# Kernel optimization log

Hardware: AMD Instinct MI355X
Metric: run time of the kernel (lower is better)

Reference implementation:

```python
import jax, jax.numpy as jnp
import numpy as np

N = 100000      # nodes (single ntype)
F_IN = 128
F_OUT = 128
R = 3           # relations
E = 262144      # edges per relation
LRELU_SLOPE = 0.2


def setup_inputs() -> dict:
    key = jax.random.key(0)
    ks = jax.random.split(key, 6)
    x = jax.random.normal(ks[0], (N, F_IN), jnp.float32)
    src = jax.random.randint(ks[1], (R, E), 0, N)
    dst = jax.random.randint(ks[2], (R, E), 0, N)
    # attention: Linear(2*in_feat, 1) per relation
    att_w = jax.random.normal(ks[3], (R, 2 * F_IN, 1), jnp.float32) * 0.05
    att_b = jnp.zeros((R, 1), jnp.float32)
    # transform: Linear(in_feat, out_feat) per relation
    tw = jax.random.normal(ks[4], (R, F_IN, F_OUT), jnp.float32) * (1.0 / np.sqrt(F_IN))
    tb = jnp.zeros((R, F_OUT), jnp.float32)
    h_bias = jnp.zeros((F_OUT,), jnp.float32)
    return dict(x=x, att_w=att_w, att_b=att_b, tw=tw, tb=tb,
                h_bias=h_bias, src=src, dst=dst)


def reference(x, att_w, att_b, tw, tb, h_bias, src, dst):
    # Per-relation gather of endpoint features.  [R, E, F_IN]
    h_src = x[src]
    h_dst = x[dst]
    # attention Linear on cat([h_src, h_dst]) == split matmul (avoids concat)
    w_s, w_d = att_w[:, :F_IN, :], att_w[:, F_IN:, :]
    scores = (jnp.einsum('ref,rfo->reo', h_src, w_s)
              + jnp.einsum('ref,rfo->reo', h_dst, w_d)
              + att_b[:, None, :])                      # [R, E, 1]
    scores = jax.nn.leaky_relu(scores, negative_slope=LRELU_SLOPE)
    # Faithful to source: F.softmax(scores, dim=0) -> softmax over ALL edges
    # of a relation (NOT per-destination edge softmax).
    a = jax.nn.softmax(scores, axis=1)                  # [R, E, 1]
    # u_mul_e with node-level transform(h_src): message = (h_src @ tw + tb) * a
    msg = (jnp.einsum('ref,rfo->reo', h_src, tw) + tb[:, None, :]) * a  # [R,E,F_OUT]
    # scatter-sum to destinations per relation, then sum over relations
    agg = jax.vmap(lambda m, d: jax.ops.segment_sum(m, d, num_segments=N))(msg, dst)
    h = agg.sum(axis=0) + h_bias                        # [N, F_OUT]
    # activation=relu, dropout=0.0 (identity)
    return jax.nn.relu(h)
```

## Files before the change

kernel.cpp:

```cpp
#include <hip/hip_runtime.h>
#include <hip/hip_bf16.h>

#define N_NODES 100000
#define FDIM 128
#define RREL 3
#define NEDGE 262144
#define SLOPE 0.2f
#define NCHUNK 98
#define PROJ_BLOCKS 782
#define HIST_BLOCKS (RREL * NEDGE / 256)

typedef __attribute__((ext_vector_type(8))) short bf16x8;
typedef __attribute__((ext_vector_type(8))) unsigned short u16x8;
typedef __attribute__((ext_vector_type(4))) float f32x4;
typedef __attribute__((ext_vector_type(4))) int i32x4;

__device__ inline unsigned short f2bf(float f) {
    __hip_bfloat16 h = __float2bfloat16(f);
    return *reinterpret_cast<unsigned short*>(&h);
}
__device__ inline float bf2f(unsigned short u) {
    unsigned int b = ((unsigned int)u) << 16;
    return __int_as_float(b);
}

#define WS_PS    0
#define WS_PD    300000
#define WS_SUMS  600000
#define WS_COUNT 600016
#define WS_ROWS  900016
#define WS_BSUM  1200016
#define WS_ESORT 1200528
#define WS_ASUM  2773392
#define WS_TWT   3073392
#define WS_TBS   3097968
#define WS_XBF   3098352
#define WS_AGGB  9498352
#define WS_RANK  28698352

__global__ __launch_bounds__(256, 4)
void proj_hist_kernel(const float* __restrict__ x,
                      const float* __restrict__ att_w,
                      float* __restrict__ ps, float* __restrict__ pd,
                      unsigned short* __restrict__ x_bf,
                      const int* __restrict__ dst, int* __restrict__ count,
                      int* __restrict__ rank) {
    if (blockIdx.x >= PROJ_BLOCKS) {
        const int b = blockIdx.x - PROJ_BLOCKS;
        const int gid = b * 256 + threadIdx.x;
        const int r = b >> 10;
        rank[gid] = atomicAdd(&count[r * N_NODES + dst[gid]], 1);
        return;
    }
    __shared__ unsigned short sX[128 * 136];
    __shared__ unsigned short sW[16 * 136];
    const int tid = threadIdx.x;
    const int row0 = blockIdx.x * 128;

#pragma unroll
    for (int i = 0; i < 8; ++i) {
        const int idx = tid + i * 256;
        const int c = idx >> 7, k = idx & 127;
        float v = 0.f;
        if (c < 3) v = att_w[c * 256 + k];
        else if (c < 6) v = att_w[(c - 3) * 256 + 128 + k];
        sW[c * 136 + k] = f2bf(v);
    }
    const int g = tid >> 5, lane = tid & 31;
#pragma unroll
    for (int it = 0; it < 16; ++it) {
        const int rrow = it * 8 + g;
        const int row = row0 + rrow;
        float4 xv = make_float4(0.f, 0.f, 0.f, 0.f);
        if (row < N_NODES) xv = *reinterpret_cast<const float4*>(x + (size_t)row * FDIM + lane * 4);
        ushort4 u;
        u.x = f2bf(xv.x); u.y = f2bf(xv.y); u.z = f2bf(xv.z); u.w = f2bf(xv.w);
        if (row < N_NODES)
            *reinterpret_cast<ushort4*>(x_bf + (size_t)row * FDIM + lane * 4) = u;
        *reinterpret_cast<ushort4*>(&sX[rrow * 136 + lane * 4]) = u;
    }
    __syncthreads();

    const int w = tid >> 6, l = tid & 63;
    const int lr = l & 15, lk = l >> 4;
    f32x4 acc[2];
    acc[0] = (f32x4){0.f, 0.f, 0.f, 0.f};
    acc[1] = (f32x4){0.f, 0.f, 0.f, 0.f};
#pragma unroll
    for (int ks = 0; ks < 4; ++ks) {
        const bf16x8 bfr = *reinterpret_cast<const bf16x8*>(&sW[lr * 136 + ks * 32 + lk * 8]);
#pragma unroll
        for (int rt = 0; rt < 2; ++rt) {
            const bf16x8 afr =
                *reinterpret_cast<const bf16x8*>(&sX[(w * 32 + rt * 16 + lr) * 136 + ks * 32 + lk * 8]);
            acc[rt] = __builtin_amdgcn_mfma_f32_16x16x32_bf16(afr, bfr, acc[rt], 0, 0, 0);
        }
    }
    if (lr < 6) {
        float* base = (lr < 3) ? (ps + lr * N_NODES) : (pd + (lr - 3) * N_NODES);
#pragma unroll
        for (int rt = 0; rt < 2; ++rt) {
            const int rowbase = row0 + w * 32 + rt * 16 + lk * 4;
#pragma unroll
            for (int j = 0; j < 4; ++j) {
                const int row = rowbase + j;
                if (row < N_NODES) base[row] = acc[rt][j];
            }
        }
    }
}

__global__ void scan1_kernel(const int* __restrict__ count, int* __restrict__ row_start,
                             int* __restrict__ bsum) {
    const int r = blockIdx.x / NCHUNK;
    const int b = blockIdx.x % NCHUNK;
    const int tid = threadIdx.x;
    const int base = b * 1024 + tid * 4;
    int v[4];
#pragma unroll
    for (int i = 0; i < 4; ++i)
        v[i] = (base + i < N_NODES) ? count[r * N_NODES + base + i] : 0;
    const int tsum = v[0] + v[1] + v[2] + v[3];
    __shared__ int sd[256];
    sd[tid] = tsum;
    __syncthreads();
    for (int off = 1; off < 256; off <<= 1) {
        const int tv = (tid >= off) ? sd[tid - off] : 0;
        __syncthreads();
        sd[tid] += tv;
        __syncthreads();
    }
    int run = sd[tid] - tsum;
#pragma unroll
    for (int i = 0; i < 4; ++i) {
        if (base + i < N_NODES) row_start[r * N_NODES + base + i] = run;
        run += v[i];
    }
    if (tid == 255) bsum[blockIdx.x] = sd[255];
}

__global__ void scan2_kernel(int* __restrict__ bsum) {
    const int r = blockIdx.x;
    const int tid = threadIdx.x;
    const int v = (tid < NCHUNK) ? bsum[r * NCHUNK + tid] : 0;
    __shared__ int sd[256];
    sd[tid] = v;
    __syncthreads();
    for (int off = 1; off < 256; off <<= 1) {
        const int tv = (tid >= off) ? sd[tid - off] : 0;
        __syncthreads();
        sd[tid] += tv;
        __syncthreads();
    }
    if (tid < NCHUNK) bsum[r * NCHUNK + tid] = sd[tid] - v;
}

__global__ void scan3_kernel(int* __restrict__ row_start, const int* __restrict__ bsum) {
    const int r = blockIdx.x / NCHUNK;
    const int b = blockIdx.x % NCHUNK;
    const int add = bsum[blockIdx.x];
    const int base = b * 1024 + threadIdx.x * 4;
#pragma unroll
    for (int i = 0; i < 4; ++i)
        if (base + i < N_NODES) row_start[r * N_NODES + base + i] += add;
}

__global__ void fill_kernel(const int* __restrict__ src, const int* __restrict__ dst,
                            const float* __restrict__ ps, const float* __restrict__ pd,
                            const float* __restrict__ att_b,
                            const int* __restrict__ row_start, const int* __restrict__ rank,
                            int2* __restrict__ edge_sorted, float* __restrict__ sums) {
    const int gid = blockIdx.x * 256 + threadIdx.x;
    const int r = blockIdx.x >> 10;
    const int s = src[gid];
    const int d = dst[gid];
    float sc = ps[r * N_NODES + s] + pd[r * N_NODES + d] + att_b[r];
    sc = sc > 0.f ? sc : SLOPE * sc;
    const float ev = __expf(sc);
    const int pos = row_start[r * N_NODES + d] + rank[gid];
    int2 pk;
    pk.x = s;
    pk.y = __float_as_int(ev);
    edge_sorted[(size_t)r * NEDGE + pos] = pk;
    float v = ev;
#pragma unroll
    for (int off = 32; off >= 1; off >>= 1) v += __shfl_xor(v, off);
    __shared__ float red[4];
    if ((threadIdx.x & 63) == 0) red[threadIdx.x >> 6] = v;
    __syncthreads();
    if (threadIdx.x == 0) {
        unsafeAtomicAdd(&sums[r], red[0] + red[1] + red[2] + red[3]);
    }
}

__global__ void cast_kernel(const float* __restrict__ tw, const float* __restrict__ tb,
                            const float* __restrict__ sums,
                            unsigned short* __restrict__ twT, float* __restrict__ tbs) {
    const int c = blockIdx.x;
    const int kk = threadIdx.x;
    const float inv = 1.0f / sums[kk >> 7];
    twT[c * 384 + kk] = f2bf(tw[kk * 128 + c] * inv);
    if (c == 0) tbs[kk] = tb[kk] * inv;
}

__global__ void agg_kernel(const int* __restrict__ row_start,
                           const int2* __restrict__ edge_sorted,
                           const unsigned short* __restrict__ x_bf,
                           unsigned short* __restrict__ aggb, float* __restrict__ asum) {
    const int lane = threadIdx.x & 15;
    const int r = blockIdx.y;
    const int n = blockIdx.x * 16 + (threadIdx.x >> 4);
    const int beg = row_start[r * N_NODES + n];
    const int end = (n == N_NODES - 1) ? NEDGE : row_start[r * N_NODES + n + 1];
    const int2* es = edge_sorted + (size_t)r * NEDGE;

    float acc[8] = {0.f, 0.f, 0.f, 0.f, 0.f, 0.f, 0.f, 0.f};
    float asacc = 0.f;

    for (int i = beg; i < end; i += 4) {
        const int rem = end - i;
        int2 pk0, pk1, pk2, pk3;
        pk0 = es[i];
        if (rem > 1) pk1 = es[i + 1];
        if (rem > 2) pk2 = es[i + 2];
        if (rem > 3) pk3 = es[i + 3];
        u16x8 xv0, xv1, xv2, xv3;
        xv0 = *reinterpret_cast<const u16x8*>(x_bf + (size_t)pk0.x * FDIM + lane * 8);
        if (rem > 1) xv1 = *reinterpret_cast<const u16x8*>(x_bf + (size_t)pk1.x * FDIM + lane * 8);
        if (rem > 2) xv2 = *reinterpret_cast<const u16x8*>(x_bf + (size_t)pk2.x * FDIM + lane * 8);
        if (rem > 3) xv3 = *reinterpret_cast<const u16x8*>(x_bf + (size_t)pk3.x * FDIM + lane * 8);
        {
            const float a = __int_as_float(pk0.y);
            asacc += a;
#pragma unroll
            for (int d = 0; d < 8; ++d) acc[d] += a * bf2f(xv0[d]);
        }
        if (rem > 1) {
            const float a = __int_as_float(pk1.y);
            asacc += a;
#pragma unroll
            for (int d = 0; d < 8; ++d) acc[d] += a * bf2f(xv1[d]);
        }
        if (rem > 2) {
            const float a = __int_as_float(pk2.y);
            asacc += a;
#pragma unroll
            for (int d = 0; d < 8; ++d) acc[d] += a * bf2f(xv2[d]);
        }
        if (rem > 3) {
            const float a = __int_as_float(pk3.y);
            asacc += a;
#pragma unroll
            for (int d = 0; d < 8; ++d) acc[d] += a * bf2f(xv3[d]);
        }
    }

    u16x8 o;
#pragma unroll
    for (int d = 0; d < 8; ++d) o[d] = f2bf(acc[d]);
    i32x4* dst4 = reinterpret_cast<i32x4*>(aggb + (size_t)n * 384 + r * FDIM + lane * 8);
    __builtin_nontemporal_store(*reinterpret_cast<i32x4*>(&o), dst4);
    if (lane == 0) asum[r * N_NODES + n] = asacc;
}

__global__ __launch_bounds__(256, 4)
void gemm_kernel(const unsigned short* __restrict__ A, const unsigned short* __restrict__ Bt,
                 const float* __restrict__ asum, const float* __restrict__ tbs,
                 const float* __restrict__ h_bias, float* __restrict__ out) {
    __shared__ unsigned short sA[2][128 * 40];
    __shared__ unsigned short sB[2][128 * 40];
    const int tid = threadIdx.x;
    const int row0 = blockIdx.x * 128;
    const int rs = tid >> 2;
    const int koff = (tid & 3) * 8;

#pragma unroll
    for (int i = 0; i < 2; ++i) {
        const int rc = rs + i * 64;
        const int grow = row0 + rc;
        int4 va = {0, 0, 0, 0};
        if (grow < N_NODES)
            va = *reinterpret_cast<const int4*>(&A[(size_t)grow * 384 + koff]);
        *reinterpret_cast<int4*>(&sA[0][rc * 40 + koff]) = va;
        const int4 vb = *reinterpret_cast<const int4*>(&Bt[rc * 384 + koff]);
        *reinterpret_cast<int4*>(&sB[0][rc * 40 + koff]) = vb;
    }
    __syncthreads();

    const int w = tid >> 6, l = tid & 63;
    const int lr = l & 15, lk = l >> 4;
    f32x4 acc[2][8];
#pragma unroll
    for (int rt = 0; rt < 2; ++rt)
#pragma unroll
        for (int ct = 0; ct < 8; ++ct) acc[rt][ct] = (f32x4){0.f, 0.f, 0.f, 0.f};

    for (int ks = 0; ks < 12; ++ks) {
        const int buf = ks & 1;
        int4 ra[2], rb[2];
        if (ks < 11) {
            const int k0 = (ks + 1) * 32;
#pragma unroll
            for (int i = 0; i < 2; ++i) {
                const int rc = rs + i * 64;
                const int grow = row0 + rc;
                ra[i] = make_int4(0, 0, 0, 0);
                if (grow < N_NODES)
                    ra[i] = *reinterpret_cast<const int4*>(&A[(size_t)grow * 384 + k0 + koff]);
                rb[i] = *reinterpret_cast<const int4*>(&Bt[rc * 384 + k0 + koff]);
            }
        }
        bf16x8 afr[2];
#pragma unroll
        for (int rt = 0; rt < 2; ++rt)
            afr[rt] = *reinterpret_cast<const bf16x8*>(&sA[buf][(w * 32 + rt * 16 + lr) * 40 + lk * 8]);
#pragma unroll
        for (int ct = 0; ct < 8; ++ct) {
            const bf16x8 bfr = *reinterpret_cast<const bf16x8*>(&sB[buf][(ct * 16 + lr) * 40 + lk * 8]);
            acc[0][ct] = __builtin_amdgcn_mfma_f32_16x16x32_bf16(afr[0], bfr, acc[0][ct], 0, 0, 0);
            acc[1][ct] = __builtin_amdgcn_mfma_f32_16x16x32_bf16(afr[1], bfr, acc[1][ct], 0, 0, 0);
        }
        if (ks < 11) {
#pragma unroll
            for (int i = 0; i < 2; ++i) {
                const int rc = rs + i * 64;
                *reinterpret_cast<int4*>(&sA[buf ^ 1][rc * 40 + koff]) = ra[i];
                *reinterpret_cast<int4*>(&sB[buf ^ 1][rc * 40 + koff]) = rb[i];
            }
        }
        __syncthreads();
    }

#pragma unroll
    for (int rt = 0; rt < 2; ++rt) {
        const int rowbase = row0 + w * 32 + rt * 16 + lk * 4;
        float as[RREL][4];
#pragma unroll
        for (int r = 0; r < RREL; ++r)
#pragma unroll
            for (int j = 0; j < 4; ++j)
                as[r][j] = (rowbase + j < N_NODES) ? asum[r * N_NODES + rowbase + j] : 0.f;
#pragma unroll
        for (int ct = 0; ct < 8; ++ct) {
            const int col = ct * 16 + lr;
            const float hb = h_bias[col];
            const float t0 = tbs[col], t1 = tbs[FDIM + col], t2 = tbs[2 * FDIM + col];
#pragma unroll
            for (int j = 0; j < 4; ++j) {
                const int row = rowbase + j;
                if (row < N_NODES) {
                    float v = acc[rt][ct][j] + as[0][j] * t0 + as[1][j] * t1 + as[2][j] * t2 + hb;
                    out[(size_t)row * FDIM + col] = fmaxf(v, 0.f);
                }
            }
        }
    }
}

extern "C" void kernel_launch(void* const* d_in, const int* in_sizes, int n_in,
                              void* d_out, int out_size, void* d_ws, size_t ws_size,
                              hipStream_t stream) {
    const float* x      = (const float*)d_in[0];
    const float* att_w  = (const float*)d_in[1];
    const float* att_b  = (const float*)d_in[2];
    const float* tw     = (const float*)d_in[3];
    const float* tb     = (const float*)d_in[4];
    const float* h_bias = (const float*)d_in[5];
    const int*   src    = (const int*)d_in[6];
    const int*   dst    = (const int*)d_in[7];
    float* out = (float*)d_out;

    float* wsf = (float*)d_ws;
    float* ps         = wsf + WS_PS;
    float* pd         = wsf + WS_PD;
    float* sums       = wsf + WS_SUMS;
    int*   count      = (int*)(wsf + WS_COUNT);
    int*   row_start  = (int*)(wsf + WS_ROWS);
    int*   bsum       = (int*)(wsf + WS_BSUM);
    int2*  edge_sorted= (int2*)(wsf + WS_ESORT);
    float* asum       = wsf + WS_ASUM;
    unsigned short* twT  = (unsigned short*)(wsf + WS_TWT);
    float* tbs        = wsf + WS_TBS;
    unsigned short* x_bf = (unsigned short*)(wsf + WS_XBF);
    unsigned short* aggb = (unsigned short*)(wsf + WS_AGGB);
    int*   rank       = (int*)(wsf + WS_RANK);

    hipMemsetAsync(sums, 0, 16 * sizeof(float), stream);
    hipMemsetAsync(count, 0, (size_t)RREL * N_NODES * sizeof(int), stream);

    proj_hist_kernel<<<PROJ_BLOCKS + HIST_BLOCKS, 256, 0, stream>>>(x, att_w, ps, pd, x_bf,
                                                                    dst, count, rank);

    scan1_kernel<<<RREL * NCHUNK, 256, 0, stream>>>(count, row_start, bsum);
    scan2_kernel<<<RREL, 256, 0, stream>>>(bsum);
    scan3_kernel<<<RREL * NCHUNK, 256, 0, stream>>>(row_start, bsum);

    fill_kernel<<<RREL * NEDGE / 256, 256, 0, stream>>>(src, dst, ps, pd, att_b,
                                                        row_start, rank, edge_sorted, sums);

    cast_kernel<<<FDIM, 384, 0, stream>>>(tw, tb, sums, twT, tbs);

    agg_kernel<<<dim3(N_NODES / 16, RREL), 256, 0, stream>>>(row_start, edge_sorted, x_bf,
                                                             aggb, asum);

    gemm_kernel<<<(N_NODES + 127) / 128, 256, 0, stream>>>(aggb, twT, asum, tbs, h_bias, out);
}
```

Measured before the change: 194.6 us.

## Drop LDS staging in GEMM, load MFMA fragments from global; nontemporal edge loads

The GEMM kernel no longer double-buffers A and B tiles through shared memory. Each wave now loads its 16-row A fragment and the B fragments straight from global memory into MFMA operands, with a 64-row block tile and a lower occupancy bound in launch_bounds. This removes the LDS traffic and barrier syncs, but the small B matrix is re-read by every wave through cache. The aggregation kernel also reads the packed edge records as 64-bit nontemporal loads to limit cache pollution from the streaming edge list.

After: 266.7 us. 37.1% more time.

```diff
diff --git a/kernel.cpp b/kernel.cpp
--- a/kernel.cpp
+++ b/kernel.cpp
@@ -212,43 +212,43 @@
     const int n = blockIdx.x * 16 + (threadIdx.x >> 4);
     const int beg = row_start[r * N_NODES + n];
     const int end = (n == N_NODES - 1) ? NEDGE : row_start[r * N_NODES + n + 1];
-    const int2* es = edge_sorted + (size_t)r * NEDGE;
+    const long long* es = (const long long*)(edge_sorted + (size_t)r * NEDGE);
 
     float acc[8] = {0.f, 0.f, 0.f, 0.f, 0.f, 0.f, 0.f, 0.f};
     float asacc = 0.f;
 
     for (int i = beg; i < end; i += 4) {
         const int rem = end - i;
-        int2 pk0, pk1, pk2, pk3;
-        pk0 = es[i];
-        if (rem > 1) pk1 = es[i + 1];
-        if (rem > 2) pk2 = es[i + 2];
-        if (rem > 3) pk3 = es[i + 3];
+        long long q0, q1, q2, q3;
+        q0 = __builtin_nontemporal_load(es + i);
+        if (rem > 1) q1 = __builtin_nontemporal_load(es + i + 1);
+        if (rem > 2) q2 = __builtin_nontemporal_load(es + i + 2);
+        if (rem > 3) q3 = __builtin_nontemporal_load(es + i + 3);
         u16x8 xv0, xv1, xv2, xv3;
-        xv0 = *reinterpret_cast<const u16x8*>(x_bf + (size_t)pk0.x * FDIM + lane * 8);
-        if (rem > 1) xv1 = *reinterpret_cast<const u16x8*>(x_bf + (size_t)pk1.x * FDIM + lane * 8);
-        if (rem > 2) xv2 = *reinterpret_cast<const u16x8*>(x_bf + (size_t)pk2.x * FDIM + lane * 8);
-        if (rem > 3) xv3 = *reinterpret_cast<const u16x8*>(x_bf + (size_t)pk3.x * FDIM + lane * 8);
+        xv0 = *reinterpret_cast<const u16x8*>(x_bf + (size_t)(int)q0 * FDIM + lane * 8);
+        if (rem > 1) xv1 = *reinterpret_cast<const u16x8*>(x_bf + (size_t)(int)q1 * FDIM + lane * 8);
+        if (rem > 2) xv2 = *reinterpret_cast<const u16x8*>(x_bf + (size_t)(int)q2 * FDIM + lane * 8);
+        if (rem > 3) xv3 = *reinterpret_cast<const u16x8*>(x_bf + (size_t)(int)q3 * FDIM + lane * 8);
         {
-            const float a = __int_as_float(pk0.y);
+            const float a = __int_as_float((int)(q0 >> 32));
             asacc += a;
 #pragma unroll
             for (int d = 0; d < 8; ++d) acc[d] += a * bf2f(xv0[d]);
         }
         if (rem > 1) {
-            const float a = __int_as_float(pk1.y);
+            const float a = __int_as_float((int)(q1 >> 32));
             asacc += a;
 #pragma unroll
             for (int d = 0; d < 8; ++d) acc[d] += a * bf2f(xv1[d]);
         }
         if (rem > 2) {
-            const float a = __int_as_float(pk2.y);
+            const float a = __int_as_float((int)(q2 >> 32));
             asacc += a;
 #pragma unroll
             for (int d = 0; d < 8; ++d) acc[d] += a * bf2f(xv2[d]);
         }
         if (rem > 3) {
-            const float a = __int_as_float(pk3.y);
+            const float a = __int_as_float((int)(q3 >> 32));
             asacc += a;
 #pragma unroll
             for (int d = 0; d < 8; ++d) acc[d] += a * bf2f(xv3[d]);
@@ -263,95 +263,50 @@
     if (lane == 0) asum[r * N_NODES + n] = asacc;
 }
 
-__global__ __launch_bounds__(256, 4)
+__global__ __launch_bounds__(256, 2)
 void gemm_kernel(const unsigned short* __restrict__ A, const unsigned short* __restrict__ Bt,
                  const float* __restrict__ asum, const float* __restrict__ tbs,
                  const float* __restrict__ h_bias, float* __restrict__ out) {
-    __shared__ unsigned short sA[2][128 * 40];
-    __shared__ unsigned short sB[2][128 * 40];
     const int tid = threadIdx.x;
-    const int row0 = blockIdx.x * 128;
-    const int rs = tid >> 2;
-    const int koff = (tid & 3) * 8;
-
-#pragma unroll
-    for (int i = 0; i < 2; ++i) {
-        const int rc = rs + i * 64;
-        const int grow = row0 + rc;
-        int4 va = {0, 0, 0, 0};
-        if (grow < N_NODES)
-            va = *reinterpret_cast<const int4*>(&A[(size_t)grow * 384 + koff]);
-        *reinterpret_cast<int4*>(&sA[0][rc * 40 + koff]) = va;
-        const int4 vb = *reinterpret_cast<const int4*>(&Bt[rc * 384 + koff]);
-        *reinterpret_cast<int4*>(&sB[0][rc * 40 + koff]) = vb;
-    }
-    __syncthreads();
-
     const int w = tid >> 6, l = tid & 63;
     const int lr = l & 15, lk = l >> 4;
-    f32x4 acc[2][8];
-#pragma unroll
-    for (int rt = 0; rt < 2; ++rt)
-#pragma unroll
-        for (int ct = 0; ct < 8; ++ct) acc[rt][ct] = (f32x4){0.f, 0.f, 0.f, 0.f};
-
+    const int n0 = blockIdx.x * 64 + w * 16;
+    const int arow = min(n0 + lr, N_NODES - 1);
+    const unsigned short* aptr = A + (size_t)arow * 384 + lk * 8;
+    const unsigned short* bptr = Bt + (size_t)lr * 384 + lk * 8;
+
+    f32x4 acc[8];
+#pragma unroll
+    for (int ct = 0; ct < 8; ++ct) acc[ct] = (f32x4){0.f, 0.f, 0.f, 0.f};
+
+#pragma unroll 2
     for (int ks = 0; ks < 12; ++ks) {
-        const int buf = ks & 1;
-        int4 ra[2], rb[2];
-        if (ks < 11) {
-            const int k0 = (ks + 1) * 32;
-#pragma unroll
-            for (int i = 0; i < 2; ++i) {
-                const int rc = rs + i * 64;
-                const int grow = row0 + rc;
-                ra[i] = make_int4(0, 0, 0, 0);
-                if (grow < N_NODES)
-                    ra[i] = *reinterpret_cast<const int4*>(&A[(size_t)grow * 384 + k0 + koff]);
-                rb[i] = *reinterpret_cast<const int4*>(&Bt[rc * 384 + k0 + koff]);
-            }
-        }
-        bf16x8 afr[2];
-#pragma unroll
-        for (int rt = 0; rt < 2; ++rt)
-            afr[rt] = *reinterpret_cast<const bf16x8*>(&sA[buf][(w * 32 + rt * 16 + lr) * 40 + lk * 8]);
+        const bf16x8 af = *reinterpret_cast<const bf16x8*>(aptr + ks * 32);
 #pragma unroll
         for (int ct = 0; ct < 8; ++ct) {
-            const bf16x8 bfr = *reinterpret_cast<const bf16x8*>(&sB[buf][(ct * 16 + lr) * 40 + lk * 8]);
-            acc[0][ct] = __builtin_amdgcn_mfma_f32_16x16x32_bf16(afr[0], bfr, acc[0][ct], 0, 0, 0);
-            acc[1][ct] = __builtin_amdgcn_mfma_f32_16x16x32_bf16(afr[1], bfr, acc[1][ct], 0, 0, 0);
-        }
-        if (ks < 11) {
-#pragma unroll
-            for (int i = 0; i < 2; ++i) {
-                const int rc = rs + i * 64;
-                *reinterpret_cast<int4*>(&sA[buf ^ 1][rc * 40 + koff]) = ra[i];
-                *reinterpret_cast<int4*>(&sB[buf ^ 1][rc * 40 + koff]) = rb[i];
-            }
-        }
-        __syncthreads();
-    }
-
-#pragma unroll
-    for (int rt = 0; rt < 2; ++rt) {
-        const int rowbase = row0 + w * 32 + rt * 16 + lk * 4;
-        float as[RREL][4];
-#pragma unroll
-        for (int r = 0; r < RREL; ++r)
-#pragma unroll
-            for (int j = 0; j < 4; ++j)
-                as[r][j] = (rowbase + j < N_NODES) ? asum[r * N_NODES + rowbase + j] : 0.f;
-#pragma unroll
-        for (int ct = 0; ct < 8; ++ct) {
-            const int col = ct * 16 + lr;
-            const float hb = h_bias[col];
-            const float t0 = tbs[col], t1 = tbs[FDIM + col], t2 = tbs[2 * FDIM + col];
-#pragma unroll
-            for (int j = 0; j < 4; ++j) {
-                const int row = rowbase + j;
-                if (row < N_NODES) {
-                    float v = acc[rt][ct][j] + as[0][j] * t0 + as[1][j] * t1 + as[2][j] * t2 + hb;
-                    out[(size_t)row * FDIM + col] = fmaxf(v, 0.f);
-                }
+            const bf16x8 bf = *reinterpret_cast<const bf16x8*>(bptr + ct * (16 * 384) + ks * 32);
+            acc[ct] = __builtin_amdgcn_mfma_f32_16x16x32_bf16(af, bf, acc[ct], 0, 0, 0);
+        }
+    }
+
+    const int rowbase = n0 + lk * 4;
+    float as[RREL][4];
+#pragma unroll
+    for (int r = 0; r < RREL; ++r)
+#pragma unroll
+        for (int j = 0; j < 4; ++j)
+            as[r][j] = (rowbase + j < N_NODES) ? asum[r * N_NODES + rowbase + j] : 0.f;
+#pragma unroll
+    for (int ct = 0; ct < 8; ++ct) {
+        const int col = ct * 16 + lr;
+        const float hb = h_bias[col];
+        const float t0 = tbs[col], t1 = tbs[FDIM + col], t2 = tbs[2 * FDIM + col];
+#pragma unroll
+        for (int j = 0; j < 4; ++j) {
+            const int row = rowbase + j;
+            if (row < N_NODES) {
+                float v = acc[ct][j] + as[0][j] * t0 + as[1][j] * t1 + as[2][j] * t2 + hb;
+                out[(size_t)row * FDIM + col] = fmaxf(v, 0.f);
             }
         }
     }
@@ -403,5 +358,5 @@
     agg_kernel<<<dim3(N_NODES / 16, RREL), 256, 0, stream>>>(row_start, edge_sorted, x_bf,
                                                              aggb, asum);
 
-    gemm_kernel<<<(N_NODES + 127) / 128, 256, 0, stream>>>(aggb, twT, asum, tbs, h_bias, out);
-}
+    gemm_kernel<<<(N_NODES + 63) / 64, 256, 0, stream>>>(aggb, twT, asum, tbs, h_bias, out);
+}
```
